# Performance work log

Hardware: AMD Instinct MI355X
Metric: run time of the kernel (lower is better)

Reference implementation:

```python
import jax, jax.numpy as jnp
import numpy as np

N_NODES = 50000
N_EDGES = 1_250_000
D_FEAT = 64


def setup_inputs() -> dict:
    key = jax.random.key(0)
    k_seq, k_rows, k_cols, k_vals = jax.random.split(key, 4)
    seq = jax.random.normal(k_seq, (1, N_NODES, D_FEAT), dtype=jnp.float32)
    rows = jnp.sort(jax.random.randint(k_rows, (N_EDGES,), 0, N_NODES, dtype=jnp.int32))
    cols = jax.random.randint(k_cols, (N_EDGES,), 0, N_NODES, dtype=jnp.int32)
    vals = jax.random.uniform(k_vals, (N_EDGES,), dtype=jnp.float32)
    return {"seq": seq, "vals": vals, "rows": rows, "cols": cols}


def reference(seq, vals, rows, cols):
    # torch.spmm(adj, seq.squeeze(0)) with adj in COO form (rows, cols, vals):
    # out[r] = sum_{e: rows[e]==r} vals[e] * seq[0, cols[e], :]
    x = jnp.squeeze(seq, 0)                      # [N, D]
    gathered = x[cols] * vals[:, None]           # [E, D] gather + scale
    out = jax.ops.segment_sum(gathered, rows, num_segments=N_NODES)  # [N, D]
    return out[None]                             # unsqueeze(0) -> [1, N, D]
```

## Files before the change

kernel.cpp:

```cpp
#include <hip/hip_runtime.h>


#define WPB 4

__global__ __launch_bounds__(256) void row_ptr_kernel(
    const int* __restrict__ rows, int* __restrict__ row_start,
    int n_edges, int n_nodes)
{
    const int e = blockIdx.x * blockDim.x + threadIdx.x;
    if (e >= n_edges) return;
    const int r    = rows[e];
    const int prev = (e == 0) ? -1 : rows[e - 1];
    for (int t = prev + 1; t <= r; ++t) row_start[t] = e;
    if (e == n_edges - 1)
        for (int t = r + 1; t <= n_nodes; ++t) row_start[t] = n_edges;
}

__global__ __launch_bounds__(256) void cvt_kernel(
    const float4* __restrict__ in, uint2* __restrict__ out, int n4)
{
    const int i = blockIdx.x * blockDim.x + threadIdx.x;
    if (i >= n4) return;
    const float4 f = in[i];
    const unsigned ux = __float_as_uint(f.x), uy = __float_as_uint(f.y);
    const unsigned uz = __float_as_uint(f.z), uw = __float_as_uint(f.w);
    const unsigned bx = (ux + 0x7FFFu + ((ux >> 16) & 1u)) >> 16;
    const unsigned by = (uy + 0x7FFFu + ((uy >> 16) & 1u)) >> 16;
    const unsigned bz = (uz + 0x7FFFu + ((uz >> 16) & 1u)) >> 16;
    const unsigned bw = (uw + 0x7FFFu + ((uw >> 16) & 1u)) >> 16;
    uint2 o;
    o.x = bx | (by << 16);
    o.y = bz | (bw << 16);
    out[i] = o;
}

__global__ __launch_bounds__(256) void spmm_kernel(
    const uint2* __restrict__ seqb,
    const float* __restrict__ vals,
    const int*   __restrict__ cols,
    const int*   __restrict__ row_start,
    float*       __restrict__ out,
    int n_nodes, int n_edges)
{
    const int lane = threadIdx.x & 63;
    const int sub  = lane >> 4;
    const int fl   = lane & 15;
    const int wave = blockIdx.x * WPB + (threadIdx.x >> 6);

    const int r = wave * 4 + sub;
    if (wave * 4 >= n_nodes) return;
    const bool valid = (r < n_nodes);

    int e = 0, e_end = 0;
    if (valid) {
        e     = row_start[r];
        e_end = row_start[r + 1];
    }

    float4 acc = make_float4(0.f, 0.f, 0.f, 0.f);

    while (__any(e < e_end)) {
        int cidx = e + fl;
        cidx = (cidx < 0) ? 0 : (cidx >= n_edges ? n_edges - 1 : cidx);
        const int   c = cols[cidx];
        const float v = vals[cidx];

        uint2 x[16];
#pragma unroll
        for (int u = 0; u < 16; ++u) {
            const int cu = __shfl(c, (sub << 4) | u);
            if (e + u < e_end)
                x[u] = seqb[(cu << 4) + fl];
        }
#pragma unroll
        for (int u = 0; u < 16; ++u) {
            const float vu = __shfl(v, (sub << 4) | u);
            if (e + u < e_end) {
                const float f0 = __uint_as_float(x[u].x << 16);
                const float f1 = __uint_as_float(x[u].x & 0xFFFF0000u);
                const float f2 = __uint_as_float(x[u].y << 16);
                const float f3 = __uint_as_float(x[u].y & 0xFFFF0000u);
                acc.x = fmaf(vu, f0, acc.x);
                acc.y = fmaf(vu, f1, acc.y);
                acc.z = fmaf(vu, f2, acc.z);
                acc.w = fmaf(vu, f3, acc.w);
            }
        }
        e += 16;
    }

    if (valid)
        ((float4*)out)[(r << 4) + fl] = acc;
}

extern "C" void kernel_launch(void* const* d_in, const int* in_sizes, int n_in,
                              void* d_out, int out_size, void* d_ws, size_t ws_size,
                              hipStream_t stream) {
    const float* seq  = (const float*)d_in[0];
    const float* vals = (const float*)d_in[1];
    const int*   rows = (const int*)d_in[2];
    const int*   cols = (const int*)d_in[3];
    float*       out  = (float*)d_out;

    const int n_edges = in_sizes[1];
    const int n_nodes = out_size / 64;

    int*   row_start = (int*)d_ws;
    size_t off       = (((size_t)(n_nodes + 1) * 4 + 255) / 256) * 256;
    uint2* seqb      = (uint2*)((char*)d_ws + off);

    {
        const int threads = 256;
        const int blocks  = (n_edges + threads - 1) / threads;
        row_ptr_kernel<<<blocks, threads, 0, stream>>>(rows, row_start,
                                                       n_edges, n_nodes);
    }
    {
        const int n4     = n_nodes * 16;
        const int blocks = (n4 + 255) / 256;
        cvt_kernel<<<blocks, 256, 0, stream>>>((const float4*)seq, seqb, n4);
    }
    {
        const int waves  = (n_nodes + 3) / 4;
        const int blocks = (waves + WPB - 1) / WPB;
        spmm_kernel<<<blocks, 256, 0, stream>>>(seqb, vals, cols,
                                                row_start, out,
                                                n_nodes, n_edges);
    }
}
```

Measured before the change: 98.64 us.

## Split feature dim into two halves with separate bf16 copies, fuse prep kernels

The conversion and row-pointer kernels are fused into one launch. The bf16 copy of seq is stored as two half-feature planes (32 features each). The SpMM kernel now uses 8 lanes per row, 8 rows per wave and two blocks per row group, one per half. Each half-plane is 3.2 MB rather than 6.4 MB, so it is more likely to stay cache-resident during random gathers. The cost is that cols, vals and row_start are read twice, there are twice as many edge iterations per lane, and nontemporal hints are added on the loads and the output store.

```diff
diff --git a/kernel.cpp b/kernel.cpp
--- a/kernel.cpp
+++ b/kernel.cpp
@@ -2,40 +2,47 @@
 
 
 #define WPB 4
+#define RPW 8
 
-__global__ __launch_bounds__(256) void row_ptr_kernel(
-    const int* __restrict__ rows, int* __restrict__ row_start,
-    int n_edges, int n_nodes)
+typedef float  f32x4 __attribute__((ext_vector_type(4)));
+
+__global__ __launch_bounds__(256) void prep_kernel(
+    const float4* __restrict__ seq,
+    uint2*        __restrict__ seqt,
+    const int*    __restrict__ rows,
+    int*          __restrict__ row_start,
+    int n_nodes, int n_edges, int cvt_blocks)
 {
-    const int e = blockIdx.x * blockDim.x + threadIdx.x;
-    if (e >= n_edges) return;
-    const int r    = rows[e];
-    const int prev = (e == 0) ? -1 : rows[e - 1];
-    for (int t = prev + 1; t <= r; ++t) row_start[t] = e;
-    if (e == n_edges - 1)
-        for (int t = r + 1; t <= n_nodes; ++t) row_start[t] = n_edges;
-}
-
-__global__ __launch_bounds__(256) void cvt_kernel(
-    const float4* __restrict__ in, uint2* __restrict__ out, int n4)
-{
-    const int i = blockIdx.x * blockDim.x + threadIdx.x;
-    if (i >= n4) return;
-    const float4 f = in[i];
-    const unsigned ux = __float_as_uint(f.x), uy = __float_as_uint(f.y);
-    const unsigned uz = __float_as_uint(f.z), uw = __float_as_uint(f.w);
-    const unsigned bx = (ux + 0x7FFFu + ((ux >> 16) & 1u)) >> 16;
-    const unsigned by = (uy + 0x7FFFu + ((uy >> 16) & 1u)) >> 16;
-    const unsigned bz = (uz + 0x7FFFu + ((uz >> 16) & 1u)) >> 16;
-    const unsigned bw = (uw + 0x7FFFu + ((uw >> 16) & 1u)) >> 16;
-    uint2 o;
-    o.x = bx | (by << 16);
-    o.y = bz | (bw << 16);
-    out[i] = o;
+    if ((int)blockIdx.x < cvt_blocks) {
+        const int t = blockIdx.x * 256 + threadIdx.x;
+        if (t >= n_nodes * 16) return;
+        const float4 f = seq[t];
+        const unsigned ux = __float_as_uint(f.x), uy = __float_as_uint(f.y);
+        const unsigned uz = __float_as_uint(f.z), uw = __float_as_uint(f.w);
+        const unsigned bx = (ux + 0x7FFFu + ((ux >> 16) & 1u)) >> 16;
+        const unsigned by = (uy + 0x7FFFu + ((uy >> 16) & 1u)) >> 16;
+        const unsigned bz = (uz + 0x7FFFu + ((uz >> 16) & 1u)) >> 16;
+        const unsigned bw = (uw + 0x7FFFu + ((uw >> 16) & 1u)) >> 16;
+        uint2 o;
+        o.x = bx | (by << 16);
+        o.y = bz | (bw << 16);
+        const int n = t >> 4;
+        const int h = (t >> 3) & 1;
+        const int q = t & 7;
+        seqt[(size_t)h * (size_t)n_nodes * 8 + n * 8 + q] = o;
+    } else {
+        const int e = (blockIdx.x - cvt_blocks) * 256 + threadIdx.x;
+        if (e >= n_edges) return;
+        const int r    = rows[e];
+        const int prev = (e == 0) ? -1 : rows[e - 1];
+        for (int t = prev + 1; t <= r; ++t) row_start[t] = e;
+        if (e == n_edges - 1)
+            for (int t = r + 1; t <= n_nodes; ++t) row_start[t] = n_edges;
+    }
 }
 
 __global__ __launch_bounds__(256) void spmm_kernel(
-    const uint2* __restrict__ seqb,
+    const uint2* __restrict__ seqt,
     const float* __restrict__ vals,
     const int*   __restrict__ cols,
     const int*   __restrict__ row_start,
@@ -43,12 +50,15 @@
     int n_nodes, int n_edges)
 {
     const int lane = threadIdx.x & 63;
-    const int sub  = lane >> 4;
-    const int fl   = lane & 15;
-    const int wave = blockIdx.x * WPB + (threadIdx.x >> 6);
+    const int sub  = lane >> 3;
+    const int fl   = lane & 7;
 
-    const int r = wave * 4 + sub;
-    if (wave * 4 >= n_nodes) return;
+    const int h      = blockIdx.x & 1;
+    const int rowblk = blockIdx.x >> 1;
+    const int wave   = rowblk * WPB + (threadIdx.x >> 6);
+
+    const int r = wave * RPW + sub;
+    if (wave * RPW >= n_nodes) return;
     const bool valid = (r < n_nodes);
 
     int e = 0, e_end = 0;
@@ -57,24 +67,26 @@
         e_end = row_start[r + 1];
     }
 
+    const uint2* __restrict__ base = seqt + (size_t)h * (size_t)n_nodes * 8;
+
     float4 acc = make_float4(0.f, 0.f, 0.f, 0.f);
 
     while (__any(e < e_end)) {
         int cidx = e + fl;
         cidx = (cidx < 0) ? 0 : (cidx >= n_edges ? n_edges - 1 : cidx);
-        const int   c = cols[cidx];
-        const float v = vals[cidx];
+        const int   c = __builtin_nontemporal_load(cols + cidx);
+        const float v = __builtin_nontemporal_load(vals + cidx);
 
-        uint2 x[16];
+        uint2 x[8];
 #pragma unroll
-        for (int u = 0; u < 16; ++u) {
-            const int cu = __shfl(c, (sub << 4) | u);
+        for (int u = 0; u < 8; ++u) {
+            const int cu = __shfl(c, (sub << 3) | u);
             if (e + u < e_end)
-                x[u] = seqb[(cu << 4) + fl];
+                x[u] = base[(cu << 3) + fl];
         }
 #pragma unroll
-        for (int u = 0; u < 16; ++u) {
-            const float vu = __shfl(v, (sub << 4) | u);
+        for (int u = 0; u < 8; ++u) {
+            const float vu = __shfl(v, (sub << 3) | u);
             if (e + u < e_end) {
                 const float f0 = __uint_as_float(x[u].x << 16);
                 const float f1 = __uint_as_float(x[u].x & 0xFFFF0000u);
@@ -86,11 +98,15 @@
                 acc.w = fmaf(vu, f3, acc.w);
             }
         }
-        e += 16;
+        e += 8;
     }
 
-    if (valid)
-        ((float4*)out)[(r << 4) + fl] = acc;
+    if (valid) {
+        f32x4 o;
+        o.x = acc.x; o.y = acc.y; o.z = acc.z; o.w = acc.w;
+        __builtin_nontemporal_store(
+            o, (f32x4*)out + ((r << 4) + (h << 3) + fl));
+    }
 }
 
 extern "C" void kernel_launch(void* const* d_in, const int* in_sizes, int n_in,
@@ -107,24 +123,19 @@
 
     int*   row_start = (int*)d_ws;
     size_t off       = (((size_t)(n_nodes + 1) * 4 + 255) / 256) * 256;
-    uint2* seqb      = (uint2*)((char*)d_ws + off);
+    uint2* seqt      = (uint2*)((char*)d_ws + off);
 
     {
-        const int threads = 256;
-        const int blocks  = (n_edges + threads - 1) / threads;
-        row_ptr_kernel<<<blocks, threads, 0, stream>>>(rows, row_start,
-                                                       n_edges, n_nodes);
+        const int cvt_blocks = (n_nodes * 16 + 255) / 256;
+        const int rp_blocks  = (n_edges + 255) / 256;
+        prep_kernel<<<cvt_blocks + rp_blocks, 256, 0, stream>>>(
+            (const float4*)seq, seqt, rows, row_start,
+            n_nodes, n_edges, cvt_blocks);
     }
     {
-        const int n4     = n_nodes * 16;
-        const int blocks = (n4 + 255) / 256;
-        cvt_kernel<<<blocks, 256, 0, stream>>>((const float4*)seq, seqb, n4);
-    }
-    {
-        const int waves  = (n_nodes + 3) / 4;
-        const int blocks = (waves + WPB - 1) / WPB;
-        spmm_kernel<<<blocks, 256, 0, stream>>>(seqb, vals, cols,
-                                                row_start, out,
-                                                n_nodes, n_edges);
+        const int rows_per_blk = WPB * RPW;
+        const int rowblks      = (n_nodes + rows_per_blk - 1) / rows_per_blk;
+        spmm_kernel<<<rowblks * 2, 256, 0, stream>>>(
+            seqt, vals, cols, row_start, out, n_nodes, n_edges);
     }
 }
```

New measurement: 111.1 us. 1.13x slower.

## Fuse prep kernels and split SpMM into two column-range passes

Applied to the files above, without the earlier changes.

Merges the row-pointer and bf16 conversion kernels into one launch. It also splits the SpMM into two passes, each gathering only from half of the node columns, so the gathered half of the bf16 feature table (about 3.2MB) stays resident in cache. The second pass reads back partial sums from the output. Non-temporal loads and stores are used for cols, vals and out so they do not pollute the cache. In exchange, the edge lists are read twice and the output is written twice with an extra read.

```diff
diff --git a/kernel.cpp b/kernel.cpp
--- a/kernel.cpp
+++ b/kernel.cpp
@@ -3,44 +3,48 @@
 
 #define WPB 4
 
-__global__ __launch_bounds__(256) void row_ptr_kernel(
-    const int* __restrict__ rows, int* __restrict__ row_start,
-    int n_edges, int n_nodes)
+typedef float f32x4 __attribute__((ext_vector_type(4)));
+
+__global__ __launch_bounds__(256) void prep_kernel(
+    const float4* __restrict__ seq,
+    uint2*        __restrict__ seqb,
+    const int*    __restrict__ rows,
+    int*          __restrict__ row_start,
+    int n_nodes, int n_edges, int cvt_blocks)
 {
-    const int e = blockIdx.x * blockDim.x + threadIdx.x;
-    if (e >= n_edges) return;
-    const int r    = rows[e];
-    const int prev = (e == 0) ? -1 : rows[e - 1];
-    for (int t = prev + 1; t <= r; ++t) row_start[t] = e;
-    if (e == n_edges - 1)
-        for (int t = r + 1; t <= n_nodes; ++t) row_start[t] = n_edges;
+    if ((int)blockIdx.x < cvt_blocks) {
+        const int t = blockIdx.x * 256 + threadIdx.x;
+        if (t >= n_nodes * 16) return;
+        const float4 f = seq[t];
+        const unsigned ux = __float_as_uint(f.x), uy = __float_as_uint(f.y);
+        const unsigned uz = __float_as_uint(f.z), uw = __float_as_uint(f.w);
+        const unsigned bx = (ux + 0x7FFFu + ((ux >> 16) & 1u)) >> 16;
+        const unsigned by = (uy + 0x7FFFu + ((uy >> 16) & 1u)) >> 16;
+        const unsigned bz = (uz + 0x7FFFu + ((uz >> 16) & 1u)) >> 16;
+        const unsigned bw = (uw + 0x7FFFu + ((uw >> 16) & 1u)) >> 16;
+        uint2 o;
+        o.x = bx | (by << 16);
+        o.y = bz | (bw << 16);
+        seqb[t] = o;
+    } else {
+        const int e = (blockIdx.x - cvt_blocks) * 256 + threadIdx.x;
+        if (e >= n_edges) return;
+        const int r    = rows[e];
+        const int prev = (e == 0) ? -1 : rows[e - 1];
+        for (int t = prev + 1; t <= r; ++t) row_start[t] = e;
+        if (e == n_edges - 1)
+            for (int t = r + 1; t <= n_nodes; ++t) row_start[t] = n_edges;
+    }
 }
 
-__global__ __launch_bounds__(256) void cvt_kernel(
-    const float4* __restrict__ in, uint2* __restrict__ out, int n4)
-{
-    const int i = blockIdx.x * blockDim.x + threadIdx.x;
-    if (i >= n4) return;
-    const float4 f = in[i];
-    const unsigned ux = __float_as_uint(f.x), uy = __float_as_uint(f.y);
-    const unsigned uz = __float_as_uint(f.z), uw = __float_as_uint(f.w);
-    const unsigned bx = (ux + 0x7FFFu + ((ux >> 16) & 1u)) >> 16;
-    const unsigned by = (uy + 0x7FFFu + ((uy >> 16) & 1u)) >> 16;
-    const unsigned bz = (uz + 0x7FFFu + ((uz >> 16) & 1u)) >> 16;
-    const unsigned bw = (uw + 0x7FFFu + ((uw >> 16) & 1u)) >> 16;
-    uint2 o;
-    o.x = bx | (by << 16);
-    o.y = bz | (bw << 16);
-    out[i] = o;
-}
-
+template <int ACC>
 __global__ __launch_bounds__(256) void spmm_kernel(
     const uint2* __restrict__ seqb,
     const float* __restrict__ vals,
     const int*   __restrict__ cols,
     const int*   __restrict__ row_start,
     float*       __restrict__ out,
-    int n_nodes, int n_edges)
+    int n_nodes, int n_edges, int clo, int chi)
 {
     const int lane = threadIdx.x & 63;
     const int sub  = lane >> 4;
@@ -58,24 +62,30 @@
     }
 
     float4 acc = make_float4(0.f, 0.f, 0.f, 0.f);
+    if (ACC && valid) {
+        const f32x4 p = __builtin_nontemporal_load(
+            (const f32x4*)out + ((r << 4) + fl));
+        acc.x = p.x; acc.y = p.y; acc.z = p.z; acc.w = p.w;
+    }
 
     while (__any(e < e_end)) {
         int cidx = e + fl;
         cidx = (cidx < 0) ? 0 : (cidx >= n_edges ? n_edges - 1 : cidx);
-        const int   c = cols[cidx];
-        const float v = vals[cidx];
+        const int   c = __builtin_nontemporal_load(cols + cidx);
+        const float v = __builtin_nontemporal_load(vals + cidx);
 
         uint2 x[16];
 #pragma unroll
         for (int u = 0; u < 16; ++u) {
             const int cu = __shfl(c, (sub << 4) | u);
-            if (e + u < e_end)
+            if ((e + u < e_end) & (cu >= clo) & (cu < chi))
                 x[u] = seqb[(cu << 4) + fl];
         }
 #pragma unroll
         for (int u = 0; u < 16; ++u) {
+            const int cu = __shfl(c, (sub << 4) | u);
             const float vu = __shfl(v, (sub << 4) | u);
-            if (e + u < e_end) {
+            if ((e + u < e_end) & (cu >= clo) & (cu < chi)) {
                 const float f0 = __uint_as_float(x[u].x << 16);
                 const float f1 = __uint_as_float(x[u].x & 0xFFFF0000u);
                 const float f2 = __uint_as_float(x[u].y << 16);
@@ -89,8 +99,11 @@
         e += 16;
     }
 
-    if (valid)
-        ((float4*)out)[(r << 4) + fl] = acc;
+    if (valid) {
+        f32x4 o;
+        o.x = acc.x; o.y = acc.y; o.z = acc.z; o.w = acc.w;
+        __builtin_nontemporal_store(o, (f32x4*)out + ((r << 4) + fl));
+    }
 }
 
 extern "C" void kernel_launch(void* const* d_in, const int* in_sizes, int n_in,
@@ -110,21 +123,19 @@
     uint2* seqb      = (uint2*)((char*)d_ws + off);
 
     {
-        const int threads = 256;
-        const int blocks  = (n_edges + threads - 1) / threads;
-        row_ptr_kernel<<<blocks, threads, 0, stream>>>(rows, row_start,
-                                                       n_edges, n_nodes);
-    }
-    {
-        const int n4     = n_nodes * 16;
-        const int blocks = (n4 + 255) / 256;
-        cvt_kernel<<<blocks, 256, 0, stream>>>((const float4*)seq, seqb, n4);
+        const int cvt_blocks = (n_nodes * 16 + 255) / 256;
+        const int rp_blocks  = (n_edges + 255) / 256;
+        prep_kernel<<<cvt_blocks + rp_blocks, 256, 0, stream>>>(
+            (const float4*)seq, seqb, rows, row_start,
+            n_nodes, n_edges, cvt_blocks);
     }
     {
         const int waves  = (n_nodes + 3) / 4;
         const int blocks = (waves + WPB - 1) / WPB;
-        spmm_kernel<<<blocks, 256, 0, stream>>>(seqb, vals, cols,
-                                                row_start, out,
-                                                n_nodes, n_edges);
+        const int nhalf  = n_nodes >> 1;
+        spmm_kernel<0><<<blocks, 256, 0, stream>>>(
+            seqb, vals, cols, row_start, out, n_nodes, n_edges, 0, nhalf);
+        spmm_kernel<1><<<blocks, 256, 0, stream>>>(
+            seqb, vals, cols, row_start, out, n_nodes, n_edges, nhalf, n_nodes);
     }
 }
```

After: 126.3 us. 1.28x slower.

## Drop bf16 conversion pass and gather fp32 features directly with half-wave rows

Applied to the files above, without the earlier changes.

Removes the separate kernel that converted seq to bf16 and instead gathers fp32 rows directly. Each wave now processes two rows with 32 lanes each loading a float2, instead of four rows with 16 lanes each loading packed bf16x4. This saves one kernel launch and a full read/write pass over the feature matrix. In exchange the gather traffic per edge doubles (256 bytes instead of 128) and twice as many waves are launched. The change also restores exact fp32 accuracy.

```diff
diff --git a/kernel.cpp b/kernel.cpp
--- a/kernel.cpp
+++ b/kernel.cpp
@@ -2,6 +2,8 @@
 
 
 #define WPB 4
+
+typedef float f32x2 __attribute__((ext_vector_type(2)));
 
 __global__ __launch_bounds__(256) void row_ptr_kernel(
     const int* __restrict__ rows, int* __restrict__ row_start,
@@ -16,26 +18,8 @@
         for (int t = r + 1; t <= n_nodes; ++t) row_start[t] = n_edges;
 }
 
-__global__ __launch_bounds__(256) void cvt_kernel(
-    const float4* __restrict__ in, uint2* __restrict__ out, int n4)
-{
-    const int i = blockIdx.x * blockDim.x + threadIdx.x;
-    if (i >= n4) return;
-    const float4 f = in[i];
-    const unsigned ux = __float_as_uint(f.x), uy = __float_as_uint(f.y);
-    const unsigned uz = __float_as_uint(f.z), uw = __float_as_uint(f.w);
-    const unsigned bx = (ux + 0x7FFFu + ((ux >> 16) & 1u)) >> 16;
-    const unsigned by = (uy + 0x7FFFu + ((uy >> 16) & 1u)) >> 16;
-    const unsigned bz = (uz + 0x7FFFu + ((uz >> 16) & 1u)) >> 16;
-    const unsigned bw = (uw + 0x7FFFu + ((uw >> 16) & 1u)) >> 16;
-    uint2 o;
-    o.x = bx | (by << 16);
-    o.y = bz | (bw << 16);
-    out[i] = o;
-}
-
 __global__ __launch_bounds__(256) void spmm_kernel(
-    const uint2* __restrict__ seqb,
+    const f32x2* __restrict__ seq,
     const float* __restrict__ vals,
     const int*   __restrict__ cols,
     const int*   __restrict__ row_start,
@@ -43,12 +27,13 @@
     int n_nodes, int n_edges)
 {
     const int lane = threadIdx.x & 63;
-    const int sub  = lane >> 4;
-    const int fl   = lane & 15;
+    const int sub  = lane >> 5;
+    const int fl   = lane & 31;
+    const int ml   = lane & 15;
     const int wave = blockIdx.x * WPB + (threadIdx.x >> 6);
 
-    const int r = wave * 4 + sub;
-    if (wave * 4 >= n_nodes) return;
+    const int r = wave * 2 + sub;
+    if (wave * 2 >= n_nodes) return;
     const bool valid = (r < n_nodes);
 
     int e = 0, e_end = 0;
@@ -57,40 +42,36 @@
         e_end = row_start[r + 1];
     }
 
-    float4 acc = make_float4(0.f, 0.f, 0.f, 0.f);
+    f32x2 acc;
+    acc.x = 0.f;
+    acc.y = 0.f;
 
     while (__any(e < e_end)) {
-        int cidx = e + fl;
-        cidx = (cidx < 0) ? 0 : (cidx >= n_edges ? n_edges - 1 : cidx);
+        int cidx = e + ml;
+        if (cidx >= n_edges) cidx = n_edges - 1;
         const int   c = cols[cidx];
         const float v = vals[cidx];
 
-        uint2 x[16];
+        f32x2 x[16];
 #pragma unroll
         for (int u = 0; u < 16; ++u) {
-            const int cu = __shfl(c, (sub << 4) | u);
+            const int cu = __shfl(c, (sub << 5) | u);
             if (e + u < e_end)
-                x[u] = seqb[(cu << 4) + fl];
+                x[u] = seq[(cu << 5) + fl];
         }
 #pragma unroll
         for (int u = 0; u < 16; ++u) {
-            const float vu = __shfl(v, (sub << 4) | u);
+            const float vu = __shfl(v, (sub << 5) | u);
             if (e + u < e_end) {
-                const float f0 = __uint_as_float(x[u].x << 16);
-                const float f1 = __uint_as_float(x[u].x & 0xFFFF0000u);
-                const float f2 = __uint_as_float(x[u].y << 16);
-                const float f3 = __uint_as_float(x[u].y & 0xFFFF0000u);
-                acc.x = fmaf(vu, f0, acc.x);
-                acc.y = fmaf(vu, f1, acc.y);
-                acc.z = fmaf(vu, f2, acc.z);
-                acc.w = fmaf(vu, f3, acc.w);
+                acc.x = fmaf(vu, x[u].x, acc.x);
+                acc.y = fmaf(vu, x[u].y, acc.y);
             }
         }
         e += 16;
     }
 
     if (valid)
-        ((float4*)out)[(r << 4) + fl] = acc;
+        ((f32x2*)out)[(r << 5) + fl] = acc;
 }
 
 extern "C" void kernel_launch(void* const* d_in, const int* in_sizes, int n_in,
@@ -105,9 +86,7 @@
     const int n_edges = in_sizes[1];
     const int n_nodes = out_size / 64;
 
-    int*   row_start = (int*)d_ws;
-    size_t off       = (((size_t)(n_nodes + 1) * 4 + 255) / 256) * 256;
-    uint2* seqb      = (uint2*)((char*)d_ws + off);
+    int* row_start = (int*)d_ws;
 
     {
         const int threads = 256;
@@ -116,15 +95,10 @@
                                                        n_edges, n_nodes);
     }
     {
-        const int n4     = n_nodes * 16;
-        const int blocks = (n4 + 255) / 256;
-        cvt_kernel<<<blocks, 256, 0, stream>>>((const float4*)seq, seqb, n4);
-    }
-    {
-        const int waves  = (n_nodes + 3) / 4;
+        const int waves  = (n_nodes + 1) / 2;
         const int blocks = (waves + WPB - 1) / WPB;
-        spmm_kernel<<<blocks, 256, 0, stream>>>(seqb, vals, cols,
-                                                row_start, out,
-                                                n_nodes, n_edges);
+        spmm_kernel<<<blocks, 256, 0, stream>>>(
+            (const f32x2*)seq, vals, cols, row_start, out,
+            n_nodes, n_edges);
     }
 }
```

Result: slower. 113.6 us (+15.1%).
